# Kernel tuning notes

Hardware: AMD Instinct MI355X
Metric: run time of the kernel (lower is better)

Reference implementation:

```python
import jax, jax.numpy as jnp
import numpy as np

N_NODES = 100000
FEATURES, HIDDEN, CLASSES = 256, 128, 32
N_EDGES = 1600000


def setup_inputs() -> dict:
    key = jax.random.key(0)
    k1, k2, k3, k4, k5 = jax.random.split(key, 5)
    x = jax.random.normal(k1, (N_NODES, FEATURES), dtype=jnp.float32)
    edge_index = jax.random.randint(k2, (2, N_EDGES), 0, N_NODES, dtype=jnp.int64)
    # GCNConv: Linear(in, out, bias=False) + separate bias added after aggregation
    s1 = 1.0 / np.sqrt(FEATURES)
    s2 = 1.0 / np.sqrt(HIDDEN)
    W1 = jax.random.uniform(k3, (FEATURES, HIDDEN), jnp.float32, -s1, s1)
    b1 = jnp.zeros((HIDDEN,), jnp.float32)
    W2 = jax.random.uniform(k4, (HIDDEN, CLASSES), jnp.float32, -s2, s2)
    b2 = jnp.zeros((CLASSES,), jnp.float32)
    return {"x": x, "W1": W1, "b1": b1, "W2": W2, "b2": b2, "edge_index": edge_index}


def _gcn_conv(x, edge_index, W, b, n_nodes):
    # PyG GCNConv with add_self_loops=False: out = D^{-1/2} A D^{-1/2} (X W) + b
    src, dst = edge_index[0], edge_index[1]
    h = x @ W  # [N, out]
    deg = jax.ops.segment_sum(jnp.ones_like(dst, dtype=h.dtype), dst, num_segments=n_nodes)
    dinv = jnp.where(deg > 0, jax.lax.rsqrt(jnp.maximum(deg, 1e-12)), 0.0)
    norm = dinv[src] * dinv[dst]  # [E]
    msgs = h[src] * norm[:, None]  # [E, out] gather + scale
    out = jax.ops.segment_sum(msgs, dst, num_segments=n_nodes)  # scatter-add
    return out + b


def reference(x, W1, b1, W2, b2, edge_index):
    h = _gcn_conv(x, edge_index, W1, b1, N_NODES)
    h = jax.nn.relu(h)
    # F.dropout(training=self.training): eval mode -> identity
    h = _gcn_conv(h, edge_index, W2, b2, N_NODES)
    return jax.nn.log_softmax(h, axis=1)
```

## Files before the change

### kernel.cpp

```cpp
#include <hip/hip_runtime.h>

typedef unsigned short u16;
typedef unsigned int   u32;
typedef __attribute__((ext_vector_type(8))) short short8;
typedef __attribute__((ext_vector_type(4))) float f32x4;
typedef __attribute__((ext_vector_type(2))) float f32x2;

constexpr int BSH = 9;
constexpr int BSZ = 1 << BSH;

__device__ inline float bf2f(u32 bits16) {
    union { u32 u; float f; } c; c.u = bits16 << 16; return c.f;
}
__device__ inline u16 f2bf(float f) {
    union { float f; u32 u; } c; c.f = f;
    return (u16)((c.u + 0x8000u) >> 16);
}
__device__ inline f32x2 up2(u32 h) {
    union { u32 u[2]; f32x2 f; } c;
    c.u[0] = h << 16;
    c.u[1] = h & 0xffff0000u;
    return c.f;
}
__device__ inline int ld_edge(const void* eb, int f64, size_t idx) {
    return f64 ? (int)((const long long*)eb)[idx] : ((const int*)eb)[idx];
}

__global__ void detect_kernel(const u32* xw, const int* ebuf_int, int* flags,
                              int* bucket_rsv, int nb, int CAP) {
    __shared__ int cnt;
    if (threadIdx.x == 0) cnt = 0;
    __syncthreads();
    u32 w = xw[threadIdx.x];
    int e = (int)((w >> 7) & 0xffu);
    if (e >= 110 && e <= 145) atomicAdd(&cnt, 1);
    int ev = ebuf_int[2 * threadIdx.x + 1];
    unsigned long long any = __ballot(ev != 0);
    if ((int)threadIdx.x < nb) bucket_rsv[threadIdx.x] = threadIdx.x * CAP;
    __syncthreads();
    if (threadIdx.x == 0) {
        flags[0] = (cnt < 192) ? 1 : 0;
        flags[1] = 0;
        flags[2] = (any == 0ULL) ? 1 : 0;
    }
}

__global__ void bconv_kernel(const void* b1, const void* b2, const int* flags,
                             float* b1f, float* b2f, int HID, int CLS) {
    int i = blockIdx.x * 256 + threadIdx.x;
    int f = flags[0];
    if (i < HID) b1f[i] = f ? ((const float*)b1)[i] : bf2f(((const u16*)b1)[i]);
    if (i < CLS) b2f[i] = f ? ((const float*)b2)[i] : bf2f(((const u16*)b2)[i]);
}

__global__ __launch_bounds__(256)
void passA_kernel(const void* eb, const int* flags, int* bucket_rsv,
                  int2* bpair, int E, int nb, int CAP) {
    __shared__ int hist[256];
    __shared__ int rbase[256];
    hist[threadIdx.x] = 0;
    __syncthreads();
    int f64 = flags[2];
    int base = blockIdx.x * 8192;
    #pragma unroll
    for (int k = 0; k < 32; ++k) {
        int e = base + k * 256 + threadIdx.x;
        if (e < E) {
            int d = ld_edge(eb, f64, (size_t)E + e);
            atomicAdd(&hist[d >> BSH], 1);
        }
    }
    __syncthreads();
    {
        int b = threadIdx.x;
        int c = (b < nb) ? hist[b] : 0;
        rbase[b] = c ? atomicAdd(&bucket_rsv[b], c) : 0;
        hist[b] = 0;
    }
    __syncthreads();
    #pragma unroll
    for (int k = 0; k < 32; ++k) {
        int e = base + k * 256 + threadIdx.x;
        if (e < E) {
            int d = ld_edge(eb, f64, (size_t)E + e);
            int s = ld_edge(eb, f64, (size_t)e);
            int bb = d >> BSH;
            int r = atomicAdd(&hist[bb], 1);
            int pos = rbase[bb] + r;
            if (pos < (bb + 1) * CAP)
                bpair[pos] = make_int2(s, d);
        }
    }
}

__global__ void fillscan_kernel(const int* bucket_rsv, int* bucket_base,
                                int* row_start, int nb, int E, int N, int CAP) {
    __shared__ int wsum[4];
    int t = threadIdx.x, lane = t & 63, wv = t >> 6;
    int v = (t < nb) ? (bucket_rsv[t] - t * CAP) : 0;
    int inc = v;
    #pragma unroll
    for (int d = 1; d < 64; d <<= 1) {
        int tmp = __shfl_up(inc, d, 64);
        if (lane >= d) inc += tmp;
    }
    if (lane == 63) wsum[wv] = inc;
    __syncthreads();
    int off = 0;
    #pragma unroll
    for (int w = 0; w < 4; ++w) if (w < wv) off += wsum[w];
    int excl = off + inc - v;
    if (t <= nb) bucket_base[t] = (t == nb) ? E : excl;
    if (t == 0) row_start[N] = E;
}

__global__ __launch_bounds__(256)
void bucketF_kernel(const int2* __restrict__ bpair, const int* __restrict__ bucket_rsv,
                    const int* __restrict__ bucket_base, float* __restrict__ dinv,
                    int* __restrict__ row_start, int* __restrict__ csr, int N, int CAP) {
    __shared__ int lcnt[BSZ];
    __shared__ int lrow[BSZ];
    __shared__ int wsum[4];
    int b = blockIdx.x, d0 = b << BSH;
    int t = threadIdx.x, lane = t & 63, wv = t >> 6;
    lcnt[2 * t] = 0; lcnt[2 * t + 1] = 0;
    __syncthreads();
    int e0 = b * CAP;
    int e1 = bucket_rsv[b];
    for (int e = e0 + t; e < e1; e += 256)
        atomicAdd(&lcnt[bpair[e].y - d0], 1);
    __syncthreads();
    int c0 = lcnt[2 * t], c1 = lcnt[2 * t + 1];
    int p = c0 + c1;
    int inc = p;
    #pragma unroll
    for (int d = 1; d < 64; d <<= 1) {
        int tmp = __shfl_up(inc, d, 64);
        if (lane >= d) inc += tmp;
    }
    if (lane == 63) wsum[wv] = inc;
    __syncthreads();
    int off = 0;
    #pragma unroll
    for (int w = 0; w < 4; ++w) if (w < wv) off += wsum[w];
    int ex0 = off + inc - p;
    int bb = bucket_base[b];
    lrow[2 * t] = ex0;
    lrow[2 * t + 1] = ex0 + c0;
    int da = d0 + 2 * t, db = d0 + 2 * t + 1;
    if (da < N) { row_start[da] = bb + ex0;      dinv[da] = c0 ? rsqrtf((float)c0) : 0.f; }
    if (db < N) { row_start[db] = bb + ex0 + c0; dinv[db] = c1 ? rsqrtf((float)c1) : 0.f; }
    lcnt[2 * t] = 0; lcnt[2 * t + 1] = 0;
    __syncthreads();
    for (int e = e0 + t; e < e1; e += 256) {
        int2 pr = bpair[e];
        int li = pr.y - d0;
        int r = atomicAdd(&lcnt[li], 1);
        csr[bb + lrow[li] + r] = pr.x;
    }
}

template<int NT, int KT, int NCOLS>
__global__ void prepack_kernel(const void* W, const int* flags, u16* pack) {
    int p = blockIdx.x * 256 + threadIdx.x;
    constexpr int TOT = NT * KT * 64 * 8;
    if (p >= TOT) return;
    int j = p & 7, lane = (p >> 3) & 63, fk = p >> 9;
    int kk = fk % KT, nt = fk / KT;
    int n = nt * 16 + (lane & 15);
    int k = kk * 32 + (lane >> 4) * 8 + j;
    u16 v = flags[0] ? f2bf(((const float*)W)[k * NCOLS + n])
                     : ((const u16*)W)[k * NCOLS + n];
    pack[p] = v;
}

template<int NT, int NTF, int KT, int G>
__global__ __launch_bounds__(256)
void gemm1_kernel(const void* __restrict__ A, const int* __restrict__ ff,
                  const u16* __restrict__ Bpack, const float* __restrict__ dinv,
                  u16* __restrict__ C, int M) {
    constexpr int K = KT * 32;
    constexpr int Ncols = NTF * 16;
    constexpr int NSPLIT = NTF / NT;
    __shared__ short8 lds[NT * KT * 64];
    const int bh = blockIdx.x % NSPLIT;
    const int bm = blockIdx.x / NSPLIT;
    for (int i = threadIdx.x; i < NT * KT * 64; i += 256) {
        int lane_ = i & 63;
        int kk = (i >> 6) % KT;
        int nt = (i >> 6) / KT;
        lds[i] = ((const short8*)Bpack)[(((bh * NT + nt) * KT) + kk) * 64 + lane_];
    }
    bool fA = (*ff != 0);
    int wave = threadIdx.x >> 6, lane = threadIdx.x & 63;
    int m0 = (bm * 4 + wave) * (16 * G);
    int q = lane >> 4, l16 = lane & 15;
    int rowc[G];
    #pragma unroll
    for (int g = 0; g < G; ++g) {
        int r = m0 + g * 16 + l16;
        rowc[g] = (r < M) ? r : (M - 1);
    }
    f32x4 acc[G][NT];
    #pragma unroll
    for (int g = 0; g < G; ++g)
        #pragma unroll
        for (int nt = 0; nt < NT; ++nt) acc[g][nt] = (f32x4){0.f, 0.f, 0.f, 0.f};

    if (fA) {
        const float* Ap[G];
        #pragma unroll
        for (int g = 0; g < G; ++g)
            Ap[g] = (const float*)A + (size_t)rowc[g] * K + q * 8;
        f32x4 raw[2][G][2];
        #pragma unroll
        for (int g = 0; g < G; ++g) {
            raw[0][g][0] = ((const f32x4*)Ap[g])[0];
            raw[0][g][1] = ((const f32x4*)Ap[g])[1];
        }
        __syncthreads();
        if (m0 >= M) return;
        #pragma unroll
        for (int kk = 0; kk < KT; ++kk) {
            const int cur = kk & 1, nxt = cur ^ 1;
            if (kk + 1 < KT) {
                #pragma unroll
                for (int g = 0; g < G; ++g) {
                    const float* p = Ap[g] + (kk + 1) * 32;
                    raw[nxt][g][0] = ((const f32x4*)p)[0];
                    raw[nxt][g][1] = ((const f32x4*)p)[1];
                }
            }
            short8 a[G];
            #pragma unroll
            for (int g = 0; g < G; ++g) {
                f32x4 v0 = raw[cur][g][0];
                f32x4 v1 = raw[cur][g][1];
                union { short8 s; u16 u[8]; } pa;
                pa.u[0] = f2bf(v0[0]); pa.u[1] = f2bf(v0[1]);
                pa.u[2] = f2bf(v0[2]); pa.u[3] = f2bf(v0[3]);
                pa.u[4] = f2bf(v1[0]); pa.u[5] = f2bf(v1[1]);
                pa.u[6] = f2bf(v1[2]); pa.u[7] = f2bf(v1[3]);
                a[g] = pa.s;
            }
            #pragma unroll
            for (int nt = 0; nt < NT; ++nt) {
                short8 b = lds[(nt * KT + kk) * 64 + lane];
                #pragma unroll
                for (int g = 0; g < G; ++g)
                    acc[g][nt] = __builtin_amdgcn_mfma_f32_16x16x32_bf16(a[g], b, acc[g][nt], 0, 0, 0);
            }
        }
    } else {
        __syncthreads();
        if (m0 >= M) return;
        #pragma unroll
        for (int kk = 0; kk < KT; ++kk) {
            short8 a[G];
            #pragma unroll
            for (int g = 0; g < G; ++g)
                a[g] = ((const short8*)((const u16*)A + (size_t)rowc[g] * K))[kk * 4 + q];
            #pragma unroll
            for (int nt = 0; nt < NT; ++nt) {
                short8 b = lds[(nt * KT + kk) * 64 + lane];
                #pragma unroll
                for (int g = 0; g < G; ++g)
                    acc[g][nt] = __builtin_amdgcn_mfma_f32_16x16x32_bf16(a[g], b, acc[g][nt], 0, 0, 0);
            }
        }
    }

    #pragma unroll
    for (int g = 0; g < G; ++g) {
        float sc[4];
        #pragma unroll
        for (int r = 0; r < 4; ++r) {
            int rr = m0 + g * 16 + q * 4 + r;
            sc[r] = dinv[(rr < M) ? rr : (M - 1)];
        }
        #pragma unroll
        for (int nt = 0; nt < NT; ++nt) {
            int col = bh * (NT * 16) + nt * 16 + l16;
            #pragma unroll
            for (int r = 0; r < 4; ++r) {
                int rrow = m0 + g * 16 + q * 4 + r;
                if (rrow < M)
                    C[(size_t)rrow * Ncols + col] = f2bf(acc[g][nt][r] * sc[r]);
            }
        }
    }
}

template<int NT, int KT, int G>
__global__ __launch_bounds__(256)
void gemm_kernel(const void* __restrict__ A, const int* __restrict__ ff,
                 const u16* __restrict__ Bpack, const float* __restrict__ dinv,
                 u16* __restrict__ C, int M) {
    constexpr int K = KT * 32;
    constexpr int Ncols = NT * 16;
    __shared__ short8 lds[NT * KT * 64];
    for (int i = threadIdx.x; i < NT * KT * 64; i += 256)
        lds[i] = ((const short8*)Bpack)[i];
    bool fA = (*ff != 0);
    __syncthreads();
    int wave = threadIdx.x >> 6, lane = threadIdx.x & 63;
    int m0 = (blockIdx.x * 4 + wave) * (16 * G);
    if (m0 >= M) return;
    int q = lane >> 4;
    int rowc[G];
    #pragma unroll
    for (int g = 0; g < G; ++g) {
        int r = m0 + g * 16 + (lane & 15);
        rowc[g] = (r < M) ? r : (M - 1);
    }
    f32x4 acc[G][NT];
    #pragma unroll
    for (int g = 0; g < G; ++g)
        #pragma unroll
        for (int nt = 0; nt < NT; ++nt) acc[g][nt] = (f32x4){0.f, 0.f, 0.f, 0.f};
    #pragma unroll
    for (int kk = 0; kk < KT; ++kk) {
        short8 a[G];
        #pragma unroll
        for (int g = 0; g < G; ++g) {
            if (fA) {
                const float* Af = (const float*)A + (size_t)rowc[g] * K + kk * 32 + q * 8;
                f32x4 v0 = ((const f32x4*)Af)[0];
                f32x4 v1 = ((const f32x4*)Af)[1];
                union { short8 s; u16 u[8]; } pa;
                pa.u[0] = f2bf(v0[0]); pa.u[1] = f2bf(v0[1]);
                pa.u[2] = f2bf(v0[2]); pa.u[3] = f2bf(v0[3]);
                pa.u[4] = f2bf(v1[0]); pa.u[5] = f2bf(v1[1]);
                pa.u[6] = f2bf(v1[2]); pa.u[7] = f2bf(v1[3]);
                a[g] = pa.s;
            } else {
                a[g] = ((const short8*)((const u16*)A + (size_t)rowc[g] * K))[kk * 4 + q];
            }
        }
        #pragma unroll
        for (int nt = 0; nt < NT; ++nt) {
            short8 b = lds[(nt * KT + kk) * 64 + lane];
            #pragma unroll
            for (int g = 0; g < G; ++g)
                acc[g][nt] = __builtin_amdgcn_mfma_f32_16x16x32_bf16(a[g], b, acc[g][nt], 0, 0, 0);
        }
    }
    #pragma unroll
    for (int g = 0; g < G; ++g) {
        float sc[4];
        #pragma unroll
        for (int r = 0; r < 4; ++r) {
            int rr = m0 + g * 16 + q * 4 + r;
            sc[r] = dinv[(rr < M) ? rr : (M - 1)];
        }
        #pragma unroll
        for (int nt = 0; nt < NT; ++nt) {
            int col = nt * 16 + (lane & 15);
            #pragma unroll
            for (int r = 0; r < 4; ++r) {
                int rrow = m0 + g * 16 + q * 4 + r;
                if (rrow < M)
                    C[(size_t)rrow * Ncols + col] = f2bf(acc[g][nt][r] * sc[r]);
            }
        }
    }
}

__global__ __launch_bounds__(256)
void agg1_kernel(const u32* __restrict__ H32, const int* __restrict__ csr,
                 const int* __restrict__ row_start, const float* __restrict__ dinv,
                 const float* __restrict__ b1f, u32* __restrict__ H1, int N) {
    int wave = threadIdx.x >> 6, lane = threadIdx.x & 63;
    int n = blockIdx.x * 4 + wave;
    if (n >= N) return;
    int s0 = row_start[n], s1 = row_start[n + 1];
    f32x2 acc = {0.f, 0.f};
    for (int base = s0; base < s1; base += 64) {
        int m = s1 - base; if (m > 64) m = 64;
        int myidx = (lane < m) ? csr[base + lane] : 0;
        int j = 0;
        for (; j + 8 <= m; j += 8) {
            int i0 = __shfl(myidx, j);
            int i1 = __shfl(myidx, j + 1);
            int i2 = __shfl(myidx, j + 2);
            int i3 = __shfl(myidx, j + 3);
            int i4 = __shfl(myidx, j + 4);
            int i5 = __shfl(myidx, j + 5);
            int i6 = __shfl(myidx, j + 6);
            int i7 = __shfl(myidx, j + 7);
            u32 h0 = H32[(size_t)i0 * 64 + lane];
            u32 h1 = H32[(size_t)i1 * 64 + lane];
            u32 h2 = H32[(size_t)i2 * 64 + lane];
            u32 h3 = H32[(size_t)i3 * 64 + lane];
            u32 h4 = H32[(size_t)i4 * 64 + lane];
            u32 h5 = H32[(size_t)i5 * 64 + lane];
            u32 h6 = H32[(size_t)i6 * 64 + lane];
            u32 h7 = H32[(size_t)i7 * 64 + lane];
            f32x2 t0 = up2(h0) + up2(h1);
            f32x2 t1 = up2(h2) + up2(h3);
            f32x2 t2 = up2(h4) + up2(h5);
            f32x2 t3 = up2(h6) + up2(h7);
            acc += (t0 + t1) + (t2 + t3);
        }
        for (; j + 4 <= m; j += 4) {
            int i0 = __shfl(myidx, j);
            int i1 = __shfl(myidx, j + 1);
            int i2 = __shfl(myidx, j + 2);
            int i3 = __shfl(myidx, j + 3);
            u32 h0 = H32[(size_t)i0 * 64 + lane];
            u32 h1 = H32[(size_t)i1 * 64 + lane];
            u32 h2 = H32[(size_t)i2 * 64 + lane];
            u32 h3 = H32[(size_t)i3 * 64 + lane];
            acc += (up2(h0) + up2(h1)) + (up2(h2) + up2(h3));
        }
        for (; j < m; ++j) {
            int s = __shfl(myidx, j);
            acc += up2(H32[(size_t)s * 64 + lane]);
        }
    }
    float wn = dinv[n];
    float v0 = fmaxf(wn * acc.x + b1f[2 * lane], 0.f);
    float v1 = fmaxf(wn * acc.y + b1f[2 * lane + 1], 0.f);
    H1[(size_t)n * 64 + lane] = (u32)f2bf(v0) | ((u32)f2bf(v1) << 16);
}

__global__ __launch_bounds__(256)
void agg2_kernel(const u32* __restrict__ H2, const int* __restrict__ csr,
                 const int* __restrict__ row_start, const float* __restrict__ dinv,
                 const float* __restrict__ b2f, const int* __restrict__ ff,
                 void* __restrict__ out, int N) {
    int wave = threadIdx.x >> 6, lane = threadIdx.x & 63;
    int n = blockIdx.x * 4 + wave;
    if (n >= N) return;
    int l16 = lane & 15, grp = lane >> 4;
    int s0 = row_start[n], s1 = row_start[n + 1];
    f32x2 acc = {0.f, 0.f};
    for (int base = s0; base < s1; base += 64) {
        int m = s1 - base; if (m > 64) m = 64;
        int myidx = (lane < m) ? csr[base + lane] : 0;
        int j = 0;
        for (; j + 8 <= m; j += 8) {
            int ia = __shfl(myidx, j + grp);
            int ib = __shfl(myidx, j + 4 + grp);
            u32 ha = H2[(size_t)ia * 16 + l16];
            u32 hb = H2[(size_t)ib * 16 + l16];
            acc += up2(ha) + up2(hb);
        }
        for (; j < m; j += 4) {
            int jj = j + grp;
            int iv = __shfl(myidx, (jj < m) ? jj : 0);
            if (jj < m) acc += up2(H2[(size_t)iv * 16 + l16]);
        }
    }
    acc.x += __shfl_xor(acc.x, 16); acc.y += __shfl_xor(acc.y, 16);
    acc.x += __shfl_xor(acc.x, 32); acc.y += __shfl_xor(acc.y, 32);
    float wn = dinv[n];
    f32x2 tot;
    tot.x = wn * acc.x + b2f[2 * l16];
    tot.y = wn * acc.y + b2f[2 * l16 + 1];
    float mx = fmaxf(tot.x, tot.y);
    #pragma unroll
    for (int msk = 8; msk; msk >>= 1) mx = fmaxf(mx, __shfl_xor(mx, msk));
    float ex = expf(tot.x - mx) + expf(tot.y - mx);
    #pragma unroll
    for (int msk = 8; msk; msk >>= 1) ex += __shfl_xor(ex, msk);
    float ls = mx + logf(ex);
    if (grp == 0) {
        if (*ff) {
            f32x2 r; r.x = tot.x - ls; r.y = tot.y - ls;
            ((f32x2*)out)[(size_t)n * 16 + l16] = r;
        } else {
            ((u32*)out)[(size_t)n * 16 + l16] =
                (u32)f2bf(tot.x - ls) | ((u32)f2bf(tot.y - ls) << 16);
        }
    }
}

extern "C" void kernel_launch(void* const* d_in, const int* in_sizes, int n_in,
                              void* d_out, int out_size, void* d_ws, size_t ws_size,
                              hipStream_t stream) {
    const void* x  = d_in[0];
    const void* W1 = d_in[1];
    const void* b1 = d_in[2];
    const void* W2 = d_in[3];
    const void* b2 = d_in[4];
    const void* eb = d_in[5];

    const int HID  = in_sizes[2];
    const int CLS  = in_sizes[4];
    const int FEAT = in_sizes[1] / HID;
    const int N    = in_sizes[0] / FEAT;
    const int E    = in_sizes[5] / 2;
    const int nb   = (N + BSZ - 1) >> BSH;
    const int CAP  = (((4 * (E / nb)) >> 10) + 2) << 10;
    (void)n_in; (void)out_size;

    char* w = (char*)d_ws;
    size_t p = 0;
    auto alloc = [&](size_t bytes) {
        size_t o = p; p = (p + bytes + 255) & ~(size_t)255; return o;
    };
    int*   flags      = (int*)  (w + alloc(32));
    int*   row_start  = (int*)  (w + alloc((size_t)(N + 1) * 4));
    int*   bucket_base= (int*)  (w + alloc(257 * 4));
    int*   bucket_rsv = (int*)  (w + alloc(256 * 4));
    int2*  bpair      = (int2*) (w + alloc((size_t)nb * CAP * 8));
    int*   csr        = (int*)  (w + alloc((size_t)E * 4));
    float* dinv       = (float*)(w + alloc((size_t)N * 4));
    float* b1f        = (float*)(w + alloc((size_t)HID * 4));
    float* b2f        = (float*)(w + alloc((size_t)CLS * 4));
    u16*   B1p        = (u16*)  (w + alloc((size_t)FEAT * HID * 2));
    u16*   B2p        = (u16*)  (w + alloc((size_t)HID * CLS * 2));
    u16*   H          = (u16*)  (w + alloc((size_t)N * HID * 2));
    u16*   H1         = (u16*)  (w + alloc((size_t)N * HID * 2));
    u16*   H2         = (u16*)  (w + alloc((size_t)N * CLS * 2));
    if (p > ws_size) return;

    detect_kernel<<<1, 256, 0, stream>>>((const u32*)x, (const int*)eb, flags,
                                         bucket_rsv, nb, CAP);
    bconv_kernel<<<1, 256, 0, stream>>>(b1, b2, flags, b1f, b2f, HID, CLS);

    passA_kernel<<<(E + 8191) / 8192, 256, 0, stream>>>(eb, flags, bucket_rsv,
                                                        bpair, E, nb, CAP);
    fillscan_kernel<<<1, 256, 0, stream>>>(bucket_rsv, bucket_base, row_start,
                                           nb, E, N, CAP);
    bucketF_kernel<<<nb, 256, 0, stream>>>(bpair, bucket_rsv, bucket_base,
                                           dinv, row_start, csr, N, CAP);

    prepack_kernel<8, 8, 128><<<(8 * 8 * 64 * 8 + 255) / 256, 256, 0, stream>>>(W1, flags, B1p);
    prepack_kernel<2, 4, 32><<<(2 * 4 * 64 * 8 + 255) / 256, 256, 0, stream>>>(W2, flags, B2p);

    gemm1_kernel<2, 8, 8, 4><<<4 * ((N + 255) / 256), 256, 0, stream>>>(x, flags, B1p, dinv, H, N);
    agg1_kernel<<<(N + 3) / 4, 256, 0, stream>>>((const u32*)H, csr, row_start, dinv, b1f,
                                                 (u32*)H1, N);
    gemm_kernel<2, 4, 2><<<(N + 127) / 128, 256, 0, stream>>>(H1, flags + 1, B2p, dinv, H2, N);
    agg2_kernel<<<(N + 3) / 4, 256, 0, stream>>>((const u32*)H2, csr, row_start, dinv, b2f,
                                                 flags, (void*)d_out, N);
}
```

Baseline: 389.8 us.

## Stage GEMM1 A tiles into LDS via async global_load_lds triple buffering

The first-layer GEMM now streams the fp32 activation tiles straight into LDS with global_load_lds into a three-stage ring buffer. It uses an XOR-swizzled layout to avoid bank conflicts and waits on explicit vmcnt counts plus barriers, replacing the register double buffering. The B-matrix copy into LDS also uses async direct loads. The tile shape changes from NT=2,G=4 to NT=4,G=2, which halves the N split so x is re-read fewer times. The LDS footprint and barrier count go up, which could reduce occupancy.

```diff
diff --git a/kernel.cpp b/kernel.cpp
--- a/kernel.cpp
+++ b/kernel.cpp
@@ -24,6 +24,11 @@
 }
 __device__ inline int ld_edge(const void* eb, int f64, size_t idx) {
     return f64 ? (int)((const long long*)eb)[idx] : ((const int*)eb)[idx];
+}
+__device__ inline void gl16(const void* g, void* l) {
+    __builtin_amdgcn_global_load_lds(
+        (const __attribute__((address_space(1))) unsigned int*)g,
+        (__attribute__((address_space(3))) unsigned int*)l, 16, 0, 0);
 }
 
 __global__ void detect_kernel(const u32* xw, const int* ebuf_int, int* flags,
@@ -182,25 +187,28 @@
     constexpr int K = KT * 32;
     constexpr int Ncols = NTF * 16;
     constexpr int NSPLIT = NTF / NT;
-    __shared__ short8 lds[NT * KT * 64];
+    constexpr int BM = 4 * 16 * G;
+    constexpr int ABUF = BM * 32 * 4;
+    constexpr int BBYTES = NT * KT * 64 * 16;
+    __shared__ __align__(16) char ldsA[3 * ABUF];
+    __shared__ short8 ldsB[NT * KT * 64];
+
     const int bh = blockIdx.x % NSPLIT;
     const int bm = blockIdx.x / NSPLIT;
-    for (int i = threadIdx.x; i < NT * KT * 64; i += 256) {
-        int lane_ = i & 63;
-        int kk = (i >> 6) % KT;
-        int nt = (i >> 6) / KT;
-        lds[i] = ((const short8*)Bpack)[(((bh * NT + nt) * KT) + kk) * 64 + lane_];
-    }
-    bool fA = (*ff != 0);
-    int wave = threadIdx.x >> 6, lane = threadIdx.x & 63;
-    int m0 = (bm * 4 + wave) * (16 * G);
-    int q = lane >> 4, l16 = lane & 15;
-    int rowc[G];
-    #pragma unroll
-    for (int g = 0; g < G; ++g) {
-        int r = m0 + g * 16 + l16;
-        rowc[g] = (r < M) ? r : (M - 1);
-    }
+    const int t  = threadIdx.x;
+
+    {
+        const char* gB = (const char*)Bpack + (size_t)bh * BBYTES;
+        char* lB = (char*)ldsB;
+        #pragma unroll
+        for (int c = 0; c < BBYTES / 4096; ++c)
+            gl16(gB + c * 4096 + t * 16, lB + c * 4096 + t * 16);
+    }
+    const bool fA = (*ff != 0);
+    const int wave = t >> 6, lane = t & 63;
+    const int m0 = (bm * 4 + wave) * (16 * G);
+    const int q = lane >> 4, l16 = lane & 15;
+
     f32x4 acc[G][NT];
     #pragma unroll
     for (int g = 0; g < G; ++g)
@@ -208,34 +216,48 @@
         for (int nt = 0; nt < NT; ++nt) acc[g][nt] = (f32x4){0.f, 0.f, 0.f, 0.f};
 
     if (fA) {
-        const float* Ap[G];
-        #pragma unroll
-        for (int g = 0; g < G; ++g)
-            Ap[g] = (const float*)A + (size_t)rowc[g] * K + q * 8;
-        f32x4 raw[2][G][2];
+        const int rb = t >> 3;
+        const int sl = t & 7;
+        const int sg = sl ^ (rb & 7);
+        const float* gp[4];
+        #pragma unroll
+        for (int c = 0; c < 4; ++c) {
+            int r = bm * BM + c * 32 + rb;
+            if (r > M - 1) r = M - 1;
+            gp[c] = (const float*)A + (size_t)r * K + sg * 4;
+        }
+        int off0[G], off1[G];
         #pragma unroll
         for (int g = 0; g < G; ++g) {
-            raw[0][g][0] = ((const f32x4*)Ap[g])[0];
-            raw[0][g][1] = ((const f32x4*)Ap[g])[1];
-        }
-        __syncthreads();
-        if (m0 >= M) return;
+            int row_l = wave * (16 * G) + g * 16 + l16;
+            int r7 = row_l & 7;
+            off0[g] = row_l * 128 + ((2 * q) ^ r7) * 16;
+            off1[g] = row_l * 128 + ((2 * q + 1) ^ r7) * 16;
+        }
+        #pragma unroll
+        for (int pj = 0; pj < 2; ++pj) {
+            char* lb = ldsA + pj * ABUF + t * 16;
+            #pragma unroll
+            for (int c = 0; c < 4; ++c)
+                gl16(gp[c] + pj * 32, lb + c * 4096);
+        }
         #pragma unroll
         for (int kk = 0; kk < KT; ++kk) {
-            const int cur = kk & 1, nxt = cur ^ 1;
-            if (kk + 1 < KT) {
+            if (kk == KT - 1) asm volatile("s_waitcnt vmcnt(0)" ::: "memory");
+            else              asm volatile("s_waitcnt vmcnt(4)" ::: "memory");
+            asm volatile("s_barrier" ::: "memory");
+            if (kk + 2 < KT) {
+                char* lb = ldsA + ((kk + 2) % 3) * ABUF + t * 16;
                 #pragma unroll
-                for (int g = 0; g < G; ++g) {
-                    const float* p = Ap[g] + (kk + 1) * 32;
-                    raw[nxt][g][0] = ((const f32x4*)p)[0];
-                    raw[nxt][g][1] = ((const f32x4*)p)[1];
-                }
-            }
+                for (int c = 0; c < 4; ++c)
+                    gl16(gp[c] + (kk + 2) * 32, lb + c * 4096);
+            }
+            const char* ab = ldsA + (kk % 3) * ABUF;
             short8 a[G];
             #pragma unroll
             for (int g = 0; g < G; ++g) {
-                f32x4 v0 = raw[cur][g][0];
-                f32x4 v1 = raw[cur][g][1];
+                f32x4 v0 = *(const f32x4*)(ab + off0[g]);
+                f32x4 v1 = *(const f32x4*)(ab + off1[g]);
                 union { short8 s; u16 u[8]; } pa;
                 pa.u[0] = f2bf(v0[0]); pa.u[1] = f2bf(v0[1]);
                 pa.u[2] = f2bf(v0[2]); pa.u[3] = f2bf(v0[3]);
@@ -245,15 +267,21 @@
             }
             #pragma unroll
             for (int nt = 0; nt < NT; ++nt) {
-                short8 b = lds[(nt * KT + kk) * 64 + lane];
+                short8 b = ldsB[(nt * KT + kk) * 64 + lane];
                 #pragma unroll
                 for (int g = 0; g < G; ++g)
                     acc[g][nt] = __builtin_amdgcn_mfma_f32_16x16x32_bf16(a[g], b, acc[g][nt], 0, 0, 0);
             }
         }
     } else {
-        __syncthreads();
-        if (m0 >= M) return;
+        asm volatile("s_waitcnt vmcnt(0)" ::: "memory");
+        asm volatile("s_barrier" ::: "memory");
+        int rowc[G];
+        #pragma unroll
+        for (int g = 0; g < G; ++g) {
+            int r = m0 + g * 16 + l16;
+            rowc[g] = (r < M) ? r : (M - 1);
+        }
         #pragma unroll
         for (int kk = 0; kk < KT; ++kk) {
             short8 a[G];
@@ -262,7 +290,7 @@
                 a[g] = ((const short8*)((const u16*)A + (size_t)rowc[g] * K))[kk * 4 + q];
             #pragma unroll
             for (int nt = 0; nt < NT; ++nt) {
-                short8 b = lds[(nt * KT + kk) * 64 + lane];
+                short8 b = ldsB[(nt * KT + kk) * 64 + lane];
                 #pragma unroll
                 for (int g = 0; g < G; ++g)
                     acc[g][nt] = __builtin_amdgcn_mfma_f32_16x16x32_bf16(a[g], b, acc[g][nt], 0, 0, 0);
@@ -530,7 +558,7 @@
     prepack_kernel<8, 8, 128><<<(8 * 8 * 64 * 8 + 255) / 256, 256, 0, stream>>>(W1, flags, B1p);
     prepack_kernel<2, 4, 32><<<(2 * 4 * 64 * 8 + 255) / 256, 256, 0, stream>>>(W2, flags, B2p);
 
-    gemm1_kernel<2, 8, 8, 4><<<4 * ((N + 255) / 256), 256, 0, stream>>>(x, flags, B1p, dinv, H, N);
+    gemm1_kernel<4, 8, 8, 2><<<2 * ((N + 127) / 128), 256, 0, stream>>>(x, flags, B1p, dinv, H, N);
     agg1_kernel<<<(N + 3) / 4, 256, 0, stream>>>((const u32*)H, csr, row_start, dinv, b1f,
                                                  (u32*)H1, N);
     gemm_kernel<2, 4, 2><<<(N + 127) / 128, 256, 0, stream>>>(H1, flags + 1, B2p, dinv, H2, N);
```

Measured after the change: 377.2 us. 3.2% less time.
